# Optimization experiments

Measured on AMD Instinct MI355X. Metric: run time of the kernel, lower is better.

## Reference

```python
import jax, jax.numpy as jnp
import numpy as np

B, N, D, C = 1, 512, 128, 128
EPS = 1e-5


def _layernorm(x, g, b):
    m = jnp.mean(x, axis=-1, keepdims=True)
    v = jnp.mean(jnp.square(x - m), axis=-1, keepdims=True)
    return (x - m) * jax.lax.rsqrt(v + EPS) * g + b


def setup_inputs() -> dict:
    key = jax.random.key(0)
    ks = jax.random.split(key, 14)
    sD = 1.0 / np.sqrt(D)
    sC = 1.0 / np.sqrt(C)

    def w(k, shape, scale):
        return jax.random.normal(k, shape, dtype=jnp.float32) * scale

    return {
        "x": jax.random.normal(ks[0], (B, N, N, D), dtype=jnp.float32),
        "ln_in_g": jnp.ones((D,), jnp.float32),
        "ln_in_b": jnp.zeros((D,), jnp.float32),
        "ln_out_g": jnp.ones((C,), jnp.float32),
        "ln_out_b": jnp.zeros((C,), jnp.float32),
        "Wl": w(ks[1], (D, C), sD), "bl": w(ks[2], (C,), 0.02),
        "Wr": w(ks[3], (D, C), sD), "br": w(ks[4], (C,), 0.02),
        "Wo": w(ks[5], (C, D), sC), "bo": w(ks[6], (D,), 0.02),
        "Wlg": w(ks[7], (D, C), sD), "blg": w(ks[8], (C,), 0.02),
        "Wrg": w(ks[9], (D, C), sD), "brg": w(ks[10], (C,), 0.02),
        "Wog": w(ks[11], (D, D), sD), "bog": w(ks[12], (D,), 0.02),
    }


def reference(x, ln_in_g, ln_in_b, ln_out_g, ln_out_b,
              Wl, bl, Wr, br, Wo, bo, Wlg, blg, Wrg, brg, Wog, bog):
    # x: [B, N, N, D] pair representation
    xn = _layernorm(x, ln_in_g, ln_in_b)
    left = jax.nn.sigmoid(xn @ Wlg + blg) * (xn @ Wl + bl)    # [B,N,N,C]
    right = jax.nn.sigmoid(xn @ Wrg + brg) * (xn @ Wr + br)   # [B,N,N,C]
    # type='out': contract over k (rows): out[b,i,j,c] = sum_k left[b,k,i,c]*right[b,k,j,c]
    out = jnp.einsum('bkic,bkjc->bijc', left, right)           # [B,N,N,C]
    out = jax.nn.sigmoid(xn @ Wog + bog) * (_layernorm(out, ln_out_g, ln_out_b) @ Wo + bo)
    return out
```

## Files before the change

kernel.cpp:

```cpp
#include <hip/hip_runtime.h>
#include <hip/hip_bf16.h>
#include <cstdint>
#include <cstddef>

typedef unsigned short u16;
typedef short bf16x8 __attribute__((ext_vector_type(8)));
typedef float f32x4 __attribute__((ext_vector_type(4)));

constexpr int Ns = 512;
constexpr int Dd = 128;
constexpr int Cc = 128;
#define EPSV 1e-5f

__device__ __forceinline__ u16 f2bf(float f){
    __hip_bfloat16 h = __float2bfloat16(f);
    return *reinterpret_cast<u16*>(&h);
}
__device__ __forceinline__ float bf2f(u16 h){
    return __uint_as_float(((uint32_t)h) << 16);
}
__device__ __forceinline__ float sigmoidf_(float x){
    return __builtin_amdgcn_rcpf(1.0f + __expf(-x));
}

__global__ void k_prep(const float* __restrict__ Wl, const float* __restrict__ Wlg,
                       const float* __restrict__ Wr, const float* __restrict__ Wrg,
                       const float* __restrict__ Wog, const float* __restrict__ Wo,
                       u16* __restrict__ Wt){
    int idx = blockIdx.x * 256 + threadIdx.x;
    if (idx >= 6 * 16384) return;
    int m = idx >> 14; int nk = idx & 16383; int n = nk >> 7; int k = nk & 127;
    const float* W = (m == 0) ? Wl : (m == 1) ? Wlg : (m == 2) ? Wr
                   : (m == 3) ? Wrg : (m == 4) ? Wog : Wo;
    Wt[idx] = f2bf(W[k * Cc + n]);
}

__global__ __launch_bounds__(256) void k1(
    const float* __restrict__ x, const float* __restrict__ g_ln, const float* __restrict__ b_ln,
    const u16* __restrict__ Wt,
    const float* __restrict__ bl, const float* __restrict__ blg,
    const float* __restrict__ br, const float* __restrict__ brg,
    const float* __restrict__ bog,
    u16* __restrict__ left, u16* __restrict__ right, u16* __restrict__ og)
{
    __shared__ u16  SB[8704];
    __shared__ float gln[128], bln[128];

    const int t   = threadIdx.x;
    const int bid = blockIdx.x;
    const int a0  = (bid >> 6) << 3;
    const int b0  = (bid & 63) << 3;
    const int w = t >> 6, l = t & 63;
    const int lrow = l & 15, g = l >> 4;
    const int nb = w * 32;
    const int orow = g << 2;
    const int kb = a0 >> 3;

    const int r = t >> 2, q = t & 3;
    const int aa = a0 + (r & 7), bb = b0 + (r >> 3);
    const float4* xrow = reinterpret_cast<const float4*>(x + ((size_t)aa * Ns + bb) * Dd);
    float4 xv[8];
#pragma unroll
    for (int i2 = 0; i2 < 8; ++i2) xv[i2] = xrow[q + 4 * i2];
    if (t < 128){ gln[t] = g_ln[t]; bln[t] = b_ln[t]; }

    float s1 = 0.f, s2 = 0.f;
#pragma unroll
    for (int i2 = 0; i2 < 8; ++i2){
        float4 v = xv[i2];
        s1 += v.x + v.y + v.z + v.w;
        s2 += v.x * v.x + v.y * v.y + v.z * v.z + v.w * v.w;
    }
    s1 += __shfl_xor(s1, 1); s1 += __shfl_xor(s1, 2);
    s2 += __shfl_xor(s2, 1); s2 += __shfl_xor(s2, 2);
    const float mm  = s1 * (1.0f / 128.0f);
    const float rsv = rsqrtf(s2 * (1.0f / 128.0f) - mm * mm + EPSV);
    __syncthreads();
#pragma unroll
    for (int i2 = 0; i2 < 8; ++i2){
        const int d = (q + 4 * i2) * 4;
        ushort4 o;
        o.x = f2bf((xv[i2].x - mm) * rsv * gln[d + 0] + bln[d + 0]);
        o.y = f2bf((xv[i2].y - mm) * rsv * gln[d + 1] + bln[d + 1]);
        o.z = f2bf((xv[i2].z - mm) * rsv * gln[d + 2] + bln[d + 2]);
        o.w = f2bf((xv[i2].w - mm) * rsv * gln[d + 3] + bln[d + 3]);
        *reinterpret_cast<ushort4*>(&SB[r * 136 + d]) = o;
    }
    __syncthreads();

    bf16x8 af[4][4];
#pragma unroll
    for (int ks = 0; ks < 4; ++ks)
#pragma unroll
        for (int rf = 0; rf < 4; ++rf)
            af[ks][rf] = *reinterpret_cast<const bf16x8*>(&SB[(rf * 16 + lrow) * 136 + ks * 32 + g * 8]);
    __syncthreads();

    const f32x4 zero4 = {0.f, 0.f, 0.f, 0.f};
    f32x4 aV[4], aG[4];

    auto GEMM1 = [&](const u16* WV, const u16* WG, int cf){
        const int col = nb + cf * 16 + lrow;
#pragma unroll
        for (int rf = 0; rf < 4; ++rf){ aV[rf] = zero4; aG[rf] = zero4; }
#pragma unroll
        for (int ks = 0; ks < 4; ++ks){
            bf16x8 bv = *reinterpret_cast<const bf16x8*>(WV + (size_t)col * 128 + ks * 32 + g * 8);
            bf16x8 bg = *reinterpret_cast<const bf16x8*>(WG + (size_t)col * 128 + ks * 32 + g * 8);
#pragma unroll
            for (int rf = 0; rf < 4; ++rf)
                aV[rf] = __builtin_amdgcn_mfma_f32_16x16x32_bf16(af[ks][rf], bv, aV[rf], 0, 0, 0);
#pragma unroll
            for (int rf = 0; rf < 4; ++rf)
                aG[rf] = __builtin_amdgcn_mfma_f32_16x16x32_bf16(af[ks][rf], bg, aG[rf], 0, 0, 0);
        }
    };
    auto STW = [&](const float* bV, const float* bG, int cf){
        const int col = nb + cf * 16 + lrow;
        const float bVv = bV[col], bGv = bG[col];
#pragma unroll
        for (int rf = 0; rf < 4; ++rf){
            ushort4 pk;
#pragma unroll
            for (int j = 0; j < 4; ++j){
                const float vv = aV[rf][j] + bVv;
                const float gg = aG[rf][j] + bGv;
                ((u16*)&pk)[j] = f2bf(sigmoidf_(gg) * vv);
            }
            *reinterpret_cast<ushort4*>(&SB[col * 68 + rf * 16 + orow]) = pk;
        }
    };
    auto STORE = [&](u16* dst){
#pragma unroll
        for (int it = 0; it < 4; ++it){
            const int cl = it * 32 + (t >> 3);
            const int s  = t & 7;
            int4 v = *reinterpret_cast<const int4*>(&SB[cl * 68 + s * 8]);
            *reinterpret_cast<int4*>(dst + (((size_t)cl * 64 + kb) * Ns + b0) * 8 + s * 8) = v;
        }
    };

    GEMM1(Wt,             Wt + 16384,     0); STW(bl, blg, 0);
    GEMM1(Wt,             Wt + 16384,     1); STW(bl, blg, 1);
    __syncthreads();
    STORE(left);
    __syncthreads();
    GEMM1(Wt + 2 * 16384, Wt + 3 * 16384, 0); STW(br, brg, 0);
    GEMM1(Wt + 2 * 16384, Wt + 3 * 16384, 1); STW(br, brg, 1);
    __syncthreads();
    STORE(right);
    __syncthreads();

    const u16* WO = Wt + (size_t)4 * 16384;
#pragma unroll 1
    for (int cf = 0; cf < 2; ++cf){
        const int col = nb + cf * 16 + lrow;
#pragma unroll
        for (int rf = 0; rf < 4; ++rf) aV[rf] = zero4;
#pragma unroll
        for (int ks = 0; ks < 4; ++ks){
            bf16x8 bv = *reinterpret_cast<const bf16x8*>(WO + (size_t)col * 128 + ks * 32 + g * 8);
#pragma unroll
            for (int rf = 0; rf < 4; ++rf)
                aV[rf] = __builtin_amdgcn_mfma_f32_16x16x32_bf16(af[ks][rf], bv, aV[rf], 0, 0, 0);
        }
        const float bOv = bog[col];
#pragma unroll
        for (int rf = 0; rf < 4; ++rf)
#pragma unroll
            for (int j = 0; j < 4; ++j){
                const int row = rf * 16 + orow + j;
                SB[row * 132 + col] = f2bf(sigmoidf_(aV[rf][j] + bOv));
            }
    }
    __syncthreads();
    const int bsub = t >> 5, c4 = (t & 31) * 4;
#pragma unroll
    for (int a = 0; a < 8; ++a){
        const int row = bsub * 8 + a;
        int2 v = *reinterpret_cast<const int2*>(&SB[row * 132 + c4]);
        *reinterpret_cast<int2*>(og + (((size_t)(a0 + a) * Ns) + (b0 + bsub)) * Cc + c4) = v;
    }
}

#define K2_LOAD(AF, BF, KS) do {                                                    \
    const size_t kbrow_ = (size_t)((KS) * 4 + lkb) * Ns;                            \
    _Pragma("unroll") for (int rf = 0; rf < 4; ++rf)                                \
        AF[rf] = *reinterpret_cast<const bf16x8*>(Lc + (kbrow_ + ib + rf * 16 + lrow) * 8); \
    _Pragma("unroll") for (int cf = 0; cf < 4; ++cf)                                \
        BF[cf] = *reinterpret_cast<const bf16x8*>(Rc + (kbrow_ + jb + cf * 16 + lrow) * 8); \
} while (0)

#define K2_MM(AF, BF) do {                                                          \
    _Pragma("unroll") for (int rf = 0; rf < 4; ++rf)                                \
    _Pragma("unroll") for (int cf = 0; cf < 4; ++cf)                                \
        acc[rf][cf] = __builtin_amdgcn_mfma_f32_16x16x32_bf16(AF[rf], BF[cf], acc[rf][cf], 0, 0, 0); \
} while (0)

__global__ __launch_bounds__(256) void k2(const u16* __restrict__ left,
                                          const u16* __restrict__ right,
                                          u16* __restrict__ om)
{
    __shared__ u16 sO[128][136];
    const int bid = blockIdx.x;
    const int xcd = bid & 7, idxx = bid >> 3;
    const int virt = xcd * 256 + idxx;
    const int c    = virt >> 4;
    const int tile = virt & 15;
    const int iy = tile >> 2, jx = tile & 3;
    const int t = threadIdx.x, w = t >> 6, l = t & 63;
    const int wr = w >> 1, wc = w & 1;
    const int ib = iy * 128 + wr * 64;
    const int jb = jx * 128 + wc * 64;
    const int lrow = l & 15, lkb = l >> 4;
    const u16* Lc = left  + (size_t)c * (Ns * Ns);
    const u16* Rc = right + (size_t)c * (Ns * Ns);
    const f32x4 zero4 = {0.f, 0.f, 0.f, 0.f};
    f32x4 acc[4][4];
#pragma unroll
    for (int rf = 0; rf < 4; ++rf)
#pragma unroll
        for (int cf = 0; cf < 4; ++cf) acc[rf][cf] = zero4;

    bf16x8 a0f[4], b0f[4], a1f[4], b1f[4];
    K2_LOAD(a0f, b0f, 0);
#pragma unroll
    for (int ks = 0; ks < 16; ks += 2){
        K2_LOAD(a1f, b1f, ks + 1);
        K2_MM(a0f, b0f);
        if (ks + 2 < 16) K2_LOAD(a0f, b0f, ks + 2);
        K2_MM(a1f, b1f);
    }

    const int orow = (l >> 4) << 2;
#pragma unroll
    for (int rf = 0; rf < 4; ++rf)
#pragma unroll
        for (int j2 = 0; j2 < 4; ++j2){
            const int rloc = wr * 64 + rf * 16 + orow + j2;
#pragma unroll
            for (int cf = 0; cf < 4; ++cf)
                sO[rloc][wc * 64 + cf * 16 + lrow] = f2bf(acc[rf][cf][j2]);
        }
    __syncthreads();
    u16* obase = om + (size_t)c * Ns * Ns + (size_t)(iy * 128) * Ns + jx * 128;
#pragma unroll
    for (int s = 0; s < 8; ++s){
        const int gg = s * 256 + t;
        const int row = gg >> 4, co = (gg & 15) * 8;
        int4 v = *reinterpret_cast<const int4*>(&sO[row][co]);
        *reinterpret_cast<int4*>(obase + (size_t)row * Ns + co) = v;
    }
}

__global__ __launch_bounds__(256) void k3(
    const u16* __restrict__ om, const u16* __restrict__ og, const u16* __restrict__ Wt,
    const float* __restrict__ g2, const float* __restrict__ b2, const float* __restrict__ bo,
    float* __restrict__ out)
{
    __shared__ char smem[34816];
    u16* X = reinterpret_cast<u16*>(smem);
    u16* O = reinterpret_cast<u16*>(smem) + 8704;
    __shared__ float sg2[128], sb2[128];
    const int i  = blockIdx.y;
    const int j0 = blockIdx.x * 64;
    const int t  = threadIdx.x;
    if (t < 128){ sg2[t] = g2[t]; sb2[t] = b2[t]; }
    {
        const int c = t >> 1, jh = (t & 1) * 32;
        const u16* src = om + (size_t)c * Ns * Ns + (size_t)i * Ns + j0 + jh;
#pragma unroll
        for (int s = 0; s < 8; ++s){
            ushort4 v = reinterpret_cast<const ushort4*>(src)[s];
            const int jj = jh + s * 4;
            X[(jj + 0) * 136 + c] = v.x; X[(jj + 1) * 136 + c] = v.y;
            X[(jj + 2) * 136 + c] = v.z; X[(jj + 3) * 136 + c] = v.w;
        }
    }
    {
        const int jj = t >> 2, qq = t & 3;
        const u16* src = og + ((size_t)i * Ns + j0 + jj) * Cc + qq * 32;
#pragma unroll
        for (int s = 0; s < 4; ++s)
            *reinterpret_cast<int4*>(&O[jj * 136 + qq * 32 + s * 8]) = reinterpret_cast<const int4*>(src)[s];
    }
    __syncthreads();
    const int r = t >> 2, q = t & 3;
    {
        float s1 = 0.f, s2v = 0.f;
#pragma unroll
        for (int e = 0; e < 32; ++e){
            const float v = bf2f(X[r * 136 + q * 32 + e]);
            s1 += v; s2v += v * v;
        }
        s1  += __shfl_xor(s1, 1);  s1  += __shfl_xor(s1, 2);
        s2v += __shfl_xor(s2v, 1); s2v += __shfl_xor(s2v, 2);
        const float mm  = s1 * (1.0f / 128.0f);
        const float rsv = rsqrtf(s2v * (1.0f / 128.0f) - mm * mm + EPSV);
#pragma unroll
        for (int e = 0; e < 32; ++e){
            const int cc = q * 32 + e;
            const float v = bf2f(X[r * 136 + cc]);
            X[r * 136 + cc] = f2bf((v - mm) * rsv * sg2[cc] + sb2[cc]);
        }
    }
    __syncthreads();
    const int w = t >> 6, l = t & 63;
    const int lrow = l & 15, lk = (l >> 4) << 3, nbv = w * 32, orow = (l >> 4) << 2;
    const u16* WO = Wt + (size_t)5 * 16384;
    const f32x4 zero4 = {0.f, 0.f, 0.f, 0.f};
    f32x4 acc[4][2];
#pragma unroll
    for (int rf = 0; rf < 4; ++rf)
#pragma unroll
        for (int cf = 0; cf < 2; ++cf) acc[rf][cf] = zero4;
#pragma unroll
    for (int ks = 0; ks < 4; ++ks){
        const int k0 = ks * 32 + lk;
        bf16x8 af[4];
#pragma unroll
        for (int rf = 0; rf < 4; ++rf)
            af[rf] = *reinterpret_cast<const bf16x8*>(&X[(rf * 16 + lrow) * 136 + k0]);
#pragma unroll
        for (int cf = 0; cf < 2; ++cf){
            bf16x8 bv = *reinterpret_cast<const bf16x8*>(WO + (size_t)(nbv + cf * 16 + lrow) * 128 + k0);
#pragma unroll
            for (int rf = 0; rf < 4; ++rf)
                acc[rf][cf] = __builtin_amdgcn_mfma_f32_16x16x32_bf16(af[rf], bv, acc[rf][cf], 0, 0, 0);
        }
    }
    float gv[2][4][4];
#pragma unroll
    for (int cf = 0; cf < 2; ++cf){
        const int cg = nbv + cf * 16 + lrow;
        const float bov = bo[cg];
#pragma unroll
        for (int rf = 0; rf < 4; ++rf)
#pragma unroll
            for (int j = 0; j < 4; ++j){
                const int row = rf * 16 + orow + j;
                gv[cf][rf][j] = bf2f(O[row * 136 + cg]) * (acc[rf][cf][j] + bov);
            }
    }
    __syncthreads();
    float* sF = reinterpret_cast<float*>(smem);
#pragma unroll
    for (int cf = 0; cf < 2; ++cf){
        const int cg = nbv + cf * 16 + lrow;
#pragma unroll
        for (int rf = 0; rf < 4; ++rf)
#pragma unroll
            for (int j = 0; j < 4; ++j){
                const int row = rf * 16 + orow + j;
                sF[row * 128 + cg] = gv[cf][rf][j];
            }
    }
    __syncthreads();
    const float4* sF4 = reinterpret_cast<const float4*>(smem);
    float* obase = out + ((size_t)i * Ns + j0) * Cc;
#pragma unroll
    for (int s = 0; s < 8; ++s){
        const int gg = s * 256 + t;
        const int row = gg >> 5, co = (gg & 31) * 4;
        float4 v = sF4[gg];
        *reinterpret_cast<float4*>(obase + (size_t)row * Cc + co) = v;
    }
}

extern "C" void kernel_launch(void* const* d_in, const int* in_sizes, int n_in,
                              void* d_out, int out_size, void* d_ws, size_t ws_size,
                              hipStream_t stream)
{
    const float* x    = (const float*)d_in[0];
    const float* ling = (const float*)d_in[1];
    const float* linb = (const float*)d_in[2];
    const float* loutg= (const float*)d_in[3];
    const float* loutb= (const float*)d_in[4];
    const float* Wl   = (const float*)d_in[5];
    const float* bl   = (const float*)d_in[6];
    const float* Wr   = (const float*)d_in[7];
    const float* br   = (const float*)d_in[8];
    const float* Wo   = (const float*)d_in[9];
    const float* bo   = (const float*)d_in[10];
    const float* Wlg  = (const float*)d_in[11];
    const float* blg  = (const float*)d_in[12];
    const float* Wrg  = (const float*)d_in[13];
    const float* brg  = (const float*)d_in[14];
    const float* Wog  = (const float*)d_in[15];
    const float* bog  = (const float*)d_in[16];

    char* ws = (char*)d_ws;
    u16* Wt = (u16*)ws;
    const size_t off = 256 * 1024;
    const size_t SZ  = (size_t)33554432 * 2;
    u16* left  = (u16*)(ws + off);
    u16* right = (u16*)(ws + off + SZ);
    u16* og    = (u16*)(ws + off + 2 * SZ);
    u16* om    = (u16*)(ws + off + 3 * SZ);

    hipLaunchKernelGGL(k_prep, dim3(384), dim3(256), 0, stream, Wl, Wlg, Wr, Wrg, Wog, Wo, Wt);
    hipLaunchKernelGGL(k1, dim3(4096), dim3(256), 0, stream,
                       x, ling, linb, Wt, bl, blg, br, brg, bog, left, right, og);
    hipLaunchKernelGGL(k2, dim3(2048), dim3(256), 0, stream, left, right, om);
    hipLaunchKernelGGL(k3, dim3(8, 512), dim3(256), 0, stream, om, og, Wt, loutg, loutb, bo, (float*)d_out);
}
```

Measured before the change: 254.1 us.

## Stage k2 operand tiles through LDS with direct global-to-LDS loads

The triangle-contraction kernel k2 no longer loads A/B fragments straight from global memory into registers per wave. Each block now cooperatively copies 128-row left and right tiles into shared memory with global_load_lds, then all four waves read their fragments from LDS. The goal is to cut redundant global traffic, since waves sharing rows or columns previously fetched the same data. In exchange there are two barriers per k-stage and no double buffering, so load latency is no longer overlapped with MFMA work.

```diff
diff --git a/kernel.cpp b/kernel.cpp
--- a/kernel.cpp
+++ b/kernel.cpp
@@ -11,6 +11,9 @@
 constexpr int Dd = 128;
 constexpr int Cc = 128;
 #define EPSV 1e-5f
+
+#define GAS __attribute__((address_space(1)))
+#define LAS __attribute__((address_space(3)))
 
 __device__ __forceinline__ u16 f2bf(float f){
     __hip_bfloat16 h = __float2bfloat16(f);
@@ -183,25 +186,11 @@
     }
 }
 
-#define K2_LOAD(AF, BF, KS) do {                                                    \
-    const size_t kbrow_ = (size_t)((KS) * 4 + lkb) * Ns;                            \
-    _Pragma("unroll") for (int rf = 0; rf < 4; ++rf)                                \
-        AF[rf] = *reinterpret_cast<const bf16x8*>(Lc + (kbrow_ + ib + rf * 16 + lrow) * 8); \
-    _Pragma("unroll") for (int cf = 0; cf < 4; ++cf)                                \
-        BF[cf] = *reinterpret_cast<const bf16x8*>(Rc + (kbrow_ + jb + cf * 16 + lrow) * 8); \
-} while (0)
-
-#define K2_MM(AF, BF) do {                                                          \
-    _Pragma("unroll") for (int rf = 0; rf < 4; ++rf)                                \
-    _Pragma("unroll") for (int cf = 0; cf < 4; ++cf)                                \
-        acc[rf][cf] = __builtin_amdgcn_mfma_f32_16x16x32_bf16(AF[rf], BF[cf], acc[rf][cf], 0, 0, 0); \
-} while (0)
-
 __global__ __launch_bounds__(256) void k2(const u16* __restrict__ left,
                                           const u16* __restrict__ right,
                                           u16* __restrict__ om)
 {
-    __shared__ u16 sO[128][136];
+    __shared__ u16 ST[17408];
     const int bid = blockIdx.x;
     const int xcd = bid & 7, idxx = bid >> 3;
     const int virt = xcd * 256 + idxx;
@@ -210,8 +199,7 @@
     const int iy = tile >> 2, jx = tile & 3;
     const int t = threadIdx.x, w = t >> 6, l = t & 63;
     const int wr = w >> 1, wc = w & 1;
-    const int ib = iy * 128 + wr * 64;
-    const int jb = jx * 128 + wc * 64;
+    const int ib0 = iy * 128, jb0 = jx * 128;
     const int lrow = l & 15, lkb = l >> 4;
     const u16* Lc = left  + (size_t)c * (Ns * Ns);
     const u16* Rc = right + (size_t)c * (Ns * Ns);
@@ -222,16 +210,53 @@
 #pragma unroll
         for (int cf = 0; cf < 4; ++cf) acc[rf][cf] = zero4;
 
-    bf16x8 a0f[4], b0f[4], a1f[4], b1f[4];
-    K2_LOAD(a0f, b0f, 0);
-#pragma unroll
-    for (int ks = 0; ks < 16; ks += 2){
-        K2_LOAD(a1f, b1f, ks + 1);
-        K2_MM(a0f, b0f);
-        if (ks + 2 < 16) K2_LOAD(a0f, b0f, ks + 2);
-        K2_MM(a1f, b1f);
-    }
-
+    auto STAGE = [&](int s){
+#pragma unroll
+        for (int it = 0; it < 4; ++it){
+            const int u = it * 256 + t;
+            const int kbl = u >> 7, row = u & 127;
+            const size_t goA = (((size_t)(s * 8 + kbl) * Ns) + ib0 + row) * 8;
+            __builtin_amdgcn_global_load_lds(
+                (const GAS uint32_t*)(const void*)(Lc + goA),
+                (LAS uint32_t*)(void*)&ST[(size_t)u * 8], 16, 0, 0);
+        }
+#pragma unroll
+        for (int it = 0; it < 4; ++it){
+            const int u = it * 256 + t;
+            const int kbl = u >> 7, row = u & 127;
+            const size_t goB = (((size_t)(s * 8 + kbl) * Ns) + jb0 + row) * 8;
+            __builtin_amdgcn_global_load_lds(
+                (const GAS uint32_t*)(const void*)(Rc + goB),
+                (LAS uint32_t*)(void*)&ST[8192 + (size_t)u * 8], 16, 0, 0);
+        }
+    };
+
+#pragma unroll 1
+    for (int s = 0; s < 8; ++s){
+        STAGE(s);
+        __syncthreads();
+#pragma unroll
+        for (int h = 0; h < 2; ++h){
+            const int kbl = h * 4 + lkb;
+            bf16x8 af[4], bfr[4];
+#pragma unroll
+            for (int rf = 0; rf < 4; ++rf)
+                af[rf] = *reinterpret_cast<const bf16x8*>(
+                    &ST[((size_t)kbl * 128 + wr * 64 + rf * 16 + lrow) * 8]);
+#pragma unroll
+            for (int cf = 0; cf < 4; ++cf)
+                bfr[cf] = *reinterpret_cast<const bf16x8*>(
+                    &ST[8192 + ((size_t)kbl * 128 + wc * 64 + cf * 16 + lrow) * 8]);
+#pragma unroll
+            for (int rf = 0; rf < 4; ++rf)
+#pragma unroll
+                for (int cf = 0; cf < 4; ++cf)
+                    acc[rf][cf] = __builtin_amdgcn_mfma_f32_16x16x32_bf16(af[rf], bfr[cf], acc[rf][cf], 0, 0, 0);
+        }
+        __syncthreads();
+    }
+
+    u16* sO = &ST[0];
     const int orow = (l >> 4) << 2;
 #pragma unroll
     for (int rf = 0; rf < 4; ++rf)
@@ -240,15 +265,15 @@
             const int rloc = wr * 64 + rf * 16 + orow + j2;
 #pragma unroll
             for (int cf = 0; cf < 4; ++cf)
-                sO[rloc][wc * 64 + cf * 16 + lrow] = f2bf(acc[rf][cf][j2]);
-        }
-    __syncthreads();
-    u16* obase = om + (size_t)c * Ns * Ns + (size_t)(iy * 128) * Ns + jx * 128;
+                sO[rloc * 136 + wc * 64 + cf * 16 + lrow] = f2bf(acc[rf][cf][j2]);
+        }
+    __syncthreads();
+    u16* obase = om + (size_t)c * Ns * Ns + (size_t)ib0 * Ns + jb0;
 #pragma unroll
     for (int s = 0; s < 8; ++s){
         const int gg = s * 256 + t;
         const int row = gg >> 4, co = (gg & 15) * 8;
-        int4 v = *reinterpret_cast<const int4*>(&sO[row][co]);
+        int4 v = *reinterpret_cast<const int4*>(&sO[row * 136 + co]);
         *reinterpret_cast<int4*>(obase + (size_t)row * Ns + co) = v;
     }
 }
```

Measured after the change: 250.4 us. About the same (-1.5%).
